# Optimization experiments

Measured on AMD Instinct MI355X. Metric: run time of the kernel, lower is better.

The kernel has to match this reference:

```python
import jax, jax.numpy as jnp
import numpy as np

B, IN, E, H, V, T = 512, 256, 256, 512, 32000, 32


def setup_inputs() -> dict:
    key = jax.random.key(0)
    ks = jax.random.split(key, 8)
    s = 0.05
    return {
        "x": jax.random.normal(ks[0], (B, IN), jnp.float32),
        "agent_w": jax.random.normal(ks[1], (H, IN), jnp.float32) * s,
        "agent_b": jnp.zeros((H,), jnp.float32),
        "sos": jax.random.normal(ks[2], (E,), jnp.float32) * 0.01,
        "emb": jax.random.normal(ks[3], (V, E), jnp.float32) * s,
        "W_ih": jax.random.normal(ks[4], (3 * H, E), jnp.float32) * s,
        "W_hh": jax.random.normal(ks[5], (3 * H, H), jnp.float32) * s,
        "b_ih": jnp.zeros((3 * H,), jnp.float32),
        "b_hh": jnp.zeros((3 * H,), jnp.float32),
        "W_out": jax.random.normal(ks[6], (V, H), jnp.float32) * s,
        "b_out": jnp.zeros((V,), jnp.float32),
        "W_stop": jax.random.normal(ks[7], (1, H), jnp.float32) * s,
        "b_stop": jnp.zeros((1,), jnp.float32),
    }


def _gru_cell(inp, h, W_ih, W_hh, b_ih, b_hh):
    gi = inp @ W_ih.T + b_ih              # [B, 3H]
    gh = h @ W_hh.T + b_hh                # [B, 3H]
    i_r, i_z, i_n = jnp.split(gi, 3, axis=1)
    h_r, h_z, h_n = jnp.split(gh, 3, axis=1)
    r = jax.nn.sigmoid(i_r + h_r)
    z = jax.nn.sigmoid(i_z + h_z)
    n = jnp.tanh(i_n + r * h_n)
    return (1.0 - z) * n + z * h


def reference(x, agent_w, agent_b, sos, emb, W_ih, W_hh, b_ih, b_hh,
              W_out, b_out, W_stop, b_stop):
    h0 = x @ agent_w.T + agent_b                       # agent(x) -> [B, H]
    inp0 = jnp.broadcast_to(sos, (x.shape[0], sos.shape[0]))
    keys = jax.random.split(jax.random.key(42), T)

    def step(carry, k):
        h, inp = carry
        h = _gru_cell(inp, h, W_ih, W_hh, b_ih, b_hh)  # noise_scale=0 -> no noise
        symb_logits = h @ W_out.T + b_out              # [B, V]
        stop_logit = (h @ W_stop.T + b_stop)[:, 0]     # [B]
        logp = jax.nn.log_softmax(symb_logits, axis=1)
        k1, k2 = jax.random.split(k)
        symb = jax.random.categorical(k1, symb_logits, axis=1)          # [B] int
        p_stop = jax.nn.sigmoid(stop_logit)
        stop = jax.random.bernoulli(k2, p_stop).astype(jnp.float32)     # [B]
        symb_lp = jnp.take_along_axis(logp, symb[:, None], axis=1)[:, 0]
        # Bernoulli: log p = s - softplus(s), log(1-p) = -softplus(s)
        sp = jax.nn.softplus(stop_logit)
        stop_lp = stop * stop_logit - sp
        symb_ent = -jnp.sum(jnp.exp(logp) * logp, axis=1)
        stop_ent = sp - stop_logit * p_stop
        inp_next = emb[symb]
        return (h, inp_next), (symb, stop, symb_lp, stop_lp, symb_ent, stop_ent)

    _, ys = jax.lax.scan(step, (h0, inp0), keys)
    symb_seq, stop_seq, symb_lp, stop_lp, symb_ent, stop_ent = ys
    # [T, B] -> [B, T]
    tr = lambda a: a.T
    return (tr(symb_seq), tr(stop_seq).astype(jnp.int32),
            tr(symb_lp), tr(stop_lp), tr(symb_ent), tr(stop_ent))
```

## Files before the change

kernel.cpp:

```cpp
#include <hip/hip_runtime.h>
#include <hip/hip_bf16.h>
#include <stdint.h>

#define JAX_PARTITIONABLE 1

#define Bz 512
#define INz 256
#define Ez 256
#define Hz 512
#define Vz 32000
#define Tz 32
#define BTz (Bz * Tz)
#define TINYF 1.17549435e-38f

typedef float otype;
__device__ __forceinline__ void store_out(otype* out, int idx, float v) {
  out[idx] = v;
}

__device__ __forceinline__ uint32_t rotl32(uint32_t x, int r) {
  return (x << r) | (x >> (32 - r));
}
__device__ __forceinline__ void threefry2x32(uint32_t k0, uint32_t k1,
                                             uint32_t x0, uint32_t x1,
                                             uint32_t& o0, uint32_t& o1) {
  const uint32_t ks2 = k0 ^ k1 ^ 0x1BD11BDAu;
  x0 += k0; x1 += k1;
#define TF_R4(a, b, c, d)                              \
  x0 += x1; x1 = rotl32(x1, a); x1 ^= x0;              \
  x0 += x1; x1 = rotl32(x1, b); x1 ^= x0;              \
  x0 += x1; x1 = rotl32(x1, c); x1 ^= x0;              \
  x0 += x1; x1 = rotl32(x1, d); x1 ^= x0;
  TF_R4(13, 15, 26, 6)  x0 += k1;  x1 += ks2 + 1u;
  TF_R4(17, 29, 16, 24) x0 += ks2; x1 += k0 + 2u;
  TF_R4(13, 15, 26, 6)  x0 += k0;  x1 += k1 + 3u;
  TF_R4(17, 29, 16, 24) x0 += k1;  x1 += ks2 + 4u;
  TF_R4(13, 15, 26, 6)  x0 += ks2; x1 += k0 + 5u;
#undef TF_R4
  o0 = x0; o1 = x1;
}
__device__ __forceinline__ uint32_t rand_bits32(uint32_t ka, uint32_t kb,
                                                uint32_t idx, uint32_t n) {
#if JAX_PARTITIONABLE
  (void)n;
  uint32_t o0, o1;
  threefry2x32(ka, kb, 0u, idx, o0, o1);
  return o0 ^ o1;
#else
  uint32_t half = n >> 1;
  uint32_t o0, o1;
  if (idx < half) { threefry2x32(ka, kb, idx, idx + half, o0, o1); return o0; }
  threefry2x32(ka, kb, idx - half, idx, o0, o1); return o1;
#endif
}
__device__ __forceinline__ float bits_to_f01(uint32_t bits) {
  return __uint_as_float((bits >> 9) | 0x3f800000u) - 1.0f;
}

__global__ void RnnSenderReinforce_36799279792759_kernel(otype* __restrict__ out,
                                                         int n, float v) {
  int i = blockIdx.x * 256 + threadIdx.x;
  if (i < n) out[i] = v;
}

__global__ void keys_kernel(uint32_t* __restrict__ keys) {
  int t = threadIdx.x;
  if (t >= Tz) return;
  uint32_t ka, kb;
#if JAX_PARTITIONABLE
  threefry2x32(0u, 42u, 0u, (uint32_t)t, ka, kb);
#else
  {
    uint32_t j0 = 2u * t, j1 = 2u * t + 1u;
    uint32_t a0, a1, b0, b1;
    if (j0 < Tz) { threefry2x32(0u, 42u, j0, j0 + Tz, a0, a1); ka = a0; }
    else         { threefry2x32(0u, 42u, j0 - Tz, j0, a0, a1); ka = a1; }
    if (j1 < Tz) { threefry2x32(0u, 42u, j1, j1 + Tz, b0, b1); kb = b0; }
    else         { threefry2x32(0u, 42u, j1 - Tz, j1, b0, b1); kb = b1; }
  }
#endif
  uint32_t o0, o1;
#if JAX_PARTITIONABLE
  threefry2x32(ka, kb, 0u, 0u, o0, o1);
  keys[t * 4 + 0] = o0; keys[t * 4 + 1] = o1;
  threefry2x32(ka, kb, 0u, 1u, o0, o1);
  keys[t * 4 + 2] = o0; keys[t * 4 + 3] = o1;
#else
  uint32_t p0, p1, q0, q1;
  threefry2x32(ka, kb, 0u, 2u, p0, p1);
  threefry2x32(ka, kb, 1u, 3u, q0, q1);
  keys[t * 4 + 0] = p0; keys[t * 4 + 1] = q0;
  keys[t * 4 + 2] = p1; keys[t * 4 + 3] = q1;
#endif
}

#define GBM 64
#define GBN 64
#define GBK 32
#define LDSS 68

__device__ __forceinline__ void gemm_bt_body(const float* __restrict__ A,
                                             const float* __restrict__ W,
                                             const float* __restrict__ bias,
                                             float* __restrict__ C,
                                             int M, int N, int K,
                                             int bx, int by,
                                             float* As, float* Bs) {
  const int tid = threadIdx.x;
  const int tx = tid & 15;
  const int ty = tid >> 4;
  const int m0 = by * GBM;
  const int n0 = bx * GBN;
  const int lr = tid >> 3;
  const int lc = (tid & 7) << 2;

  float acc[4][4] = {};
  const float* Ap = A + (size_t)(m0 + lr) * K + lc;
  const float* Wp = W + (size_t)(n0 + lr) * K + lc;
  const size_t rstep = (size_t)32 * K;

  for (int k0 = 0; k0 < K; k0 += GBK) {
    float4 a0 = *(const float4*)(Ap + k0);
    float4 a1 = *(const float4*)(Ap + k0 + rstep);
    float4 b0 = *(const float4*)(Wp + k0);
    float4 b1 = *(const float4*)(Wp + k0 + rstep);
    __syncthreads();
    As[(lc + 0) * LDSS + lr] = a0.x;
    As[(lc + 1) * LDSS + lr] = a0.y;
    As[(lc + 2) * LDSS + lr] = a0.z;
    As[(lc + 3) * LDSS + lr] = a0.w;
    As[(lc + 0) * LDSS + lr + 32] = a1.x;
    As[(lc + 1) * LDSS + lr + 32] = a1.y;
    As[(lc + 2) * LDSS + lr + 32] = a1.z;
    As[(lc + 3) * LDSS + lr + 32] = a1.w;
    Bs[(lc + 0) * LDSS + lr] = b0.x;
    Bs[(lc + 1) * LDSS + lr] = b0.y;
    Bs[(lc + 2) * LDSS + lr] = b0.z;
    Bs[(lc + 3) * LDSS + lr] = b0.w;
    Bs[(lc + 0) * LDSS + lr + 32] = b1.x;
    Bs[(lc + 1) * LDSS + lr + 32] = b1.y;
    Bs[(lc + 2) * LDSS + lr + 32] = b1.z;
    Bs[(lc + 3) * LDSS + lr + 32] = b1.w;
    __syncthreads();
#pragma unroll
    for (int kk = 0; kk < GBK; kk++) {
      float4 af = *(const float4*)&As[kk * LDSS + (ty << 2)];
      float4 bf = *(const float4*)&Bs[kk * LDSS + (tx << 2)];
      float ar[4] = {af.x, af.y, af.z, af.w};
      float br[4] = {bf.x, bf.y, bf.z, bf.w};
#pragma unroll
      for (int i = 0; i < 4; i++)
#pragma unroll
        for (int j = 0; j < 4; j++)
          acc[i][j] = fmaf(ar[i], br[j], acc[i][j]);
    }
  }

  const int nc = n0 + (tx << 2);
  float4 bv;
  bv.x = bias[nc + 0]; bv.y = bias[nc + 1]; bv.z = bias[nc + 2]; bv.w = bias[nc + 3];
#pragma unroll
  for (int i = 0; i < 4; i++) {
    int m = m0 + (ty << 2) + i;
    float4 o;
    o.x = acc[i][0] + bv.x;
    o.y = acc[i][1] + bv.y;
    o.z = acc[i][2] + bv.z;
    o.w = acc[i][3] + bv.w;
    *(float4*)(C + (size_t)m * N + nc) = o;
  }
}

__global__ __launch_bounds__(256) void gemm_bt(const float* __restrict__ A,
                                               const float* __restrict__ W,
                                               const float* __restrict__ bias,
                                               float* __restrict__ C,
                                               int M, int N, int K) {
  __shared__ __align__(16) float As[GBK * LDSS];
  __shared__ __align__(16) float Bs[GBK * LDSS];
  gemm_bt_body(A, W, bias, C, M, N, K, blockIdx.x, blockIdx.y, As, Bs);
}

__global__ __launch_bounds__(256) void gru2_kernel(const float* __restrict__ inp,
                                                   const float* __restrict__ Wih,
                                                   const float* __restrict__ bih,
                                                   float* __restrict__ gi,
                                                   const float* __restrict__ h,
                                                   const float* __restrict__ Whh,
                                                   const float* __restrict__ bhh,
                                                   float* __restrict__ gh) {
  __shared__ __align__(16) float As[GBK * LDSS];
  __shared__ __align__(16) float Bs[GBK * LDSS];
  if (blockIdx.z == 0)
    gemm_bt_body(inp, Wih, bih, gi, Bz, 3 * Hz, Ez, blockIdx.x, blockIdx.y, As, Bs);
  else
    gemm_bt_body(h, Whh, bhh, gh, Bz, 3 * Hz, Hz, blockIdx.x, blockIdx.y, As, Bs);
}

#define QBM 256
#define QBN 128
#define QBK 32
#define QLDA 260
#define QLDB 132

__global__ __launch_bounds__(512, 4) void gemm256_bt(const float* __restrict__ A,
                                                     const float* __restrict__ W,
                                                     const float* __restrict__ bias,
                                                     float* __restrict__ C,
                                                     int M, int N, int K) {
  __shared__ __align__(16) float As[QBK * QLDA];
  __shared__ __align__(16) float Bs[QBK * QLDB];
  const int tid = threadIdx.x;
  const int tx = tid & 15;
  const int ty = tid >> 4;

  const int nP = N / QBN;
  const int G = nP >> 3;
  const int lim = G << 4;
  int b = blockIdx.x;
  int P, mi;
  if (b < lim) {
    int g = b >> 4, r = b & 15;
    mi = r >> 3;
    P = (g << 3) + (r & 7);
  } else {
    int e = b - lim;
    P = (G << 3) + (e & 1);
    mi = e >> 1;
  }
  const int m0 = mi * QBM;
  const int n0 = P * QBN;

  const int ar = tid >> 1;
  const int ak = (tid & 1) << 4;
  const int br = tid >> 2;
  const int bk = (tid & 3) << 2;

  const float* Ap = A + (size_t)(m0 + ar) * K + ak;
  const float* Wp = W + (size_t)(n0 + br) * K + bk;

  float4 a0 = *(const float4*)(Ap);
  float4 a1 = *(const float4*)(Ap + 4);
  float4 a2 = *(const float4*)(Ap + 8);
  float4 a3 = *(const float4*)(Ap + 12);
  float4 b0 = *(const float4*)(Wp);
  float4 b1 = *(const float4*)(Wp + 16);

  float acc[8][8] = {};

  for (int k0 = 0; k0 < K; k0 += QBK) {
    __syncthreads();
    As[(ak + 0) * QLDA + ar] = a0.x;
    As[(ak + 1) * QLDA + ar] = a0.y;
    As[(ak + 2) * QLDA + ar] = a0.z;
    As[(ak + 3) * QLDA + ar] = a0.w;
    As[(ak + 4) * QLDA + ar] = a1.x;
    As[(ak + 5) * QLDA + ar] = a1.y;
    As[(ak + 6) * QLDA + ar] = a1.z;
    As[(ak + 7) * QLDA + ar] = a1.w;
    As[(ak + 8) * QLDA + ar] = a2.x;
    As[(ak + 9) * QLDA + ar] = a2.y;
    As[(ak + 10) * QLDA + ar] = a2.z;
    As[(ak + 11) * QLDA + ar] = a2.w;
    As[(ak + 12) * QLDA + ar] = a3.x;
    As[(ak + 13) * QLDA + ar] = a3.y;
    As[(ak + 14) * QLDA + ar] = a3.z;
    As[(ak + 15) * QLDA + ar] = a3.w;
    Bs[(bk + 0) * QLDB + br] = b0.x;
    Bs[(bk + 1) * QLDB + br] = b0.y;
    Bs[(bk + 2) * QLDB + br] = b0.z;
    Bs[(bk + 3) * QLDB + br] = b0.w;
    Bs[(16 + bk + 0) * QLDB + br] = b1.x;
    Bs[(16 + bk + 1) * QLDB + br] = b1.y;
    Bs[(16 + bk + 2) * QLDB + br] = b1.z;
    Bs[(16 + bk + 3) * QLDB + br] = b1.w;
    __syncthreads();
    if (k0 + QBK < K) {
      a0 = *(const float4*)(Ap + k0 + QBK);
      a1 = *(const float4*)(Ap + k0 + QBK + 4);
      a2 = *(const float4*)(Ap + k0 + QBK + 8);
      a3 = *(const float4*)(Ap + k0 + QBK + 12);
      b0 = *(const float4*)(Wp + k0 + QBK);
      b1 = *(const float4*)(Wp + k0 + QBK + 16);
    }
#pragma unroll 4
    for (int kk = 0; kk < QBK; kk++) {
      float4 xa0 = *(const float4*)&As[kk * QLDA + (ty << 2)];
      float4 xa1 = *(const float4*)&As[kk * QLDA + 128 + (ty << 2)];
      float4 xb0 = *(const float4*)&Bs[kk * QLDB + (tx << 2)];
      float4 xb1 = *(const float4*)&Bs[kk * QLDB + 64 + (tx << 2)];
      float ar8[8] = {xa0.x, xa0.y, xa0.z, xa0.w, xa1.x, xa1.y, xa1.z, xa1.w};
      float br8[8] = {xb0.x, xb0.y, xb0.z, xb0.w, xb1.x, xb1.y, xb1.z, xb1.w};
#pragma unroll
      for (int i = 0; i < 8; i++)
#pragma unroll
        for (int j = 0; j < 8; j++)
          acc[i][j] = fmaf(ar8[i], br8[j], acc[i][j]);
    }
  }

  const int nc0 = n0 + (tx << 2);
  const float4 bv0 = *(const float4*)(bias + nc0);
  const float4 bv1 = *(const float4*)(bias + nc0 + 64);
#pragma unroll
  for (int hf = 0; hf < 2; hf++) {
#pragma unroll
    for (int i = 0; i < 4; i++) {
      const int m = m0 + hf * 128 + (ty << 2) + i;
      float* Cp = C + (size_t)m * N + nc0;
      float4 o;
      o.x = acc[hf * 4 + i][0] + bv0.x;
      o.y = acc[hf * 4 + i][1] + bv0.y;
      o.z = acc[hf * 4 + i][2] + bv0.z;
      o.w = acc[hf * 4 + i][3] + bv0.w;
      *(float4*)Cp = o;
      float4 o2;
      o2.x = acc[hf * 4 + i][4] + bv1.x;
      o2.y = acc[hf * 4 + i][5] + bv1.y;
      o2.z = acc[hf * 4 + i][6] + bv1.z;
      o2.w = acc[hf * 4 + i][7] + bv1.w;
      *(float4*)(Cp + 64) = o2;
    }
  }
}

__global__ void gates_kernel(const float* __restrict__ gi,
                             const float* __restrict__ gh,
                             float* __restrict__ h) {
  int idx = blockIdx.x * 256 + threadIdx.x;
  int b = idx >> 9;
  int j = idx & 511;
  const float* gib = gi + (size_t)b * (3 * Hz);
  const float* ghb = gh + (size_t)b * (3 * Hz);
  float ir = gib[j], iz = gib[j + Hz], in_ = gib[j + 2 * Hz];
  float hr = ghb[j], hz = ghb[j + Hz], hn = ghb[j + 2 * Hz];
  float r = 1.0f / (1.0f + expf(-(ir + hr)));
  float z = 1.0f / (1.0f + expf(-(iz + hz)));
  float n = tanhf(in_ + r * hn);
  float hv = h[idx];
  h[idx] = (1.0f - z) * n + z * hv;
}

__global__ __launch_bounds__(256) void stop_kernel(const float* __restrict__ h,
                                                   const float* __restrict__ W_stop,
                                                   const float* __restrict__ b_stop,
                                                   const uint32_t* __restrict__ keys,
                                                   int t, otype* __restrict__ out) {
  int wave = threadIdx.x >> 6;
  int lane = threadIdx.x & 63;
  int b = blockIdx.x * 4 + wave;
  const float* hb = h + (size_t)b * Hz;
  float s = 0.0f;
  for (int k = lane; k < Hz; k += 64) s = fmaf(hb[k], W_stop[k], s);
#pragma unroll
  for (int off = 32; off; off >>= 1) s += __shfl_down(s, off, 64);
  if (lane == 0) {
    s += b_stop[0];
    uint32_t bits = rand_bits32(keys[t * 4 + 2], keys[t * 4 + 3], (uint32_t)b, Bz);
    float u = bits_to_f01(bits);
    float p = 1.0f / (1.0f + expf(-s));
    float stop = (u < p) ? 1.0f : 0.0f;
    float sp = fmaxf(s, 0.0f) + log1pf(expf(-fabsf(s)));
    store_out(out, 1 * BTz + b * Tz + t, stop);
    store_out(out, 3 * BTz + b * Tz + t, stop * s - sp);
    store_out(out, 5 * BTz + b * Tz + t, sp - s * p);
  }
}

__global__ __launch_bounds__(256) void sample_kernel(const float* __restrict__ logits,
                                                     const uint32_t* __restrict__ keys,
                                                     int t, otype* __restrict__ out,
                                                     int* __restrict__ symb_i) {
  __shared__ float sm[256], sg[256], sgl[256], sz[256], ss[256];
  __shared__ int sgi[256];
  const int tid = threadIdx.x;
  const int b = blockIdx.x;
  const float* lb = logits + (size_t)b * Vz;
  const uint32_t k1a = keys[t * 4 + 0], k1b = keys[t * 4 + 1];
  const uint32_t base = (uint32_t)b * (uint32_t)Vz;

  float m = -INFINITY, gbest = -INFINITY, glogit = 0.0f;
  int gidx = 0x7FFFFFFF;
  for (int v = tid; v < Vz; v += 256) {
    float l = lb[v];
    m = fmaxf(m, l);
    uint32_t bits = rand_bits32(k1a, k1b, base + (uint32_t)v, (uint32_t)Bz * Vz);
    float f = bits_to_f01(bits);
    float u = fmaxf(TINYF, f + TINYF);
    float g = -logf(-logf(u));
    float val = l + g;
    if (val > gbest) { gbest = val; gidx = v; glogit = l; }
  }
  sm[tid] = m; sg[tid] = gbest; sgi[tid] = gidx; sgl[tid] = glogit;
  __syncthreads();
  for (int s2 = 128; s2; s2 >>= 1) {
    if (tid < s2) {
      sm[tid] = fmaxf(sm[tid], sm[tid + s2]);
      float go = sg[tid + s2]; int io = sgi[tid + s2];
      if (go > sg[tid] || (go == sg[tid] && io < sgi[tid])) {
        sg[tid] = go; sgi[tid] = io; sgl[tid] = sgl[tid + s2];
      }
    }
    __syncthreads();
  }
  const float M = sm[0];

  float Z = 0.0f, S1 = 0.0f;
  for (int v = tid; v < Vz; v += 256) {
    float sft = lb[v] - M;
    float e = expf(sft);
    Z += e;
    S1 = fmaf(e, sft, S1);
  }
  sz[tid] = Z; ss[tid] = S1;
  __syncthreads();
  for (int s2 = 128; s2; s2 >>= 1) {
    if (tid < s2) { sz[tid] += sz[tid + s2]; ss[tid] += ss[tid + s2]; }
    __syncthreads();
  }
  if (tid == 0) {
    float Zt = sz[0], S1t = ss[0];
    float lse = logf(Zt);
    int symb = sgi[0];
    store_out(out, 0 * BTz + b * Tz + t, (float)symb);
    store_out(out, 2 * BTz + b * Tz + t, (sgl[0] - M) - lse);
    store_out(out, 4 * BTz + b * Tz + t, lse - S1t / Zt);
    symb_i[b] = symb;
  }
}

__global__ void init_inp_kernel(float* __restrict__ inp, const float* __restrict__ sos) {
  inp[blockIdx.x * Ez + threadIdx.x] = sos[threadIdx.x];
}
__global__ void gather_kernel(const float* __restrict__ emb,
                              const int* __restrict__ symb_i,
                              float* __restrict__ inp) {
  int b = blockIdx.x;
  int s = symb_i[b];
  s = (s < 0) ? 0 : ((s >= Vz) ? (Vz - 1) : s);
  inp[(size_t)b * Ez + threadIdx.x] = emb[(size_t)s * Ez + threadIdx.x];
}

extern "C" __attribute__((visibility("default")))
void kernel_launch(void* const* d_in, const int* in_sizes, int n_in,
                   void* d_out, int out_size, void* d_ws, size_t ws_size,
                   hipStream_t stream) {
  const float* x       = (const float*)d_in[0];
  const float* agent_w = (const float*)d_in[1];
  const float* agent_b = (const float*)d_in[2];
  const float* sos     = (const float*)d_in[3];
  const float* emb     = (const float*)d_in[4];
  const float* W_ih    = (const float*)d_in[5];
  const float* W_hh    = (const float*)d_in[6];
  const float* b_ih    = (const float*)d_in[7];
  const float* b_hh    = (const float*)d_in[8];
  const float* W_out   = (const float*)d_in[9];
  const float* b_out   = (const float*)d_in[10];
  const float* W_stop  = (const float*)d_in[11];
  const float* b_stop  = (const float*)d_in[12];
  otype* out = (otype*)d_out;

  float* ws = (float*)d_ws;
  float* h      = ws;
  float* inp    = h + (size_t)Bz * Hz;
  float* gi     = inp + (size_t)Bz * Ez;
  float* gh     = gi + (size_t)Bz * 3 * Hz;
  float* logits = gh + (size_t)Bz * 3 * Hz;
  int* symb_i   = (int*)(logits + (size_t)Bz * Vz);
  uint32_t* keys = (uint32_t*)(symb_i + Bz);

  keys_kernel<<<1, 64, 0, stream>>>(keys);
  init_inp_kernel<<<Bz, Ez, 0, stream>>>(inp, sos);
  gemm_bt<<<dim3(Hz / GBN, Bz / GBM), 256, 0, stream>>>(x, agent_w, agent_b, h,
                                                        Bz, Hz, INz);
  for (int t = 0; t < Tz; t++) {
    gru2_kernel<<<dim3(3 * Hz / GBN, Bz / GBM, 2), 256, 0, stream>>>(
        inp, W_ih, b_ih, gi, h, W_hh, b_hh, gh);
    gates_kernel<<<(Bz * Hz) / 256, 256, 0, stream>>>(gi, gh, h);
    gemm256_bt<<<(Vz / QBN) * (Bz / QBM), 512, 0, stream>>>(h, W_out, b_out,
                                                            logits, Bz, Vz, Hz);
    stop_kernel<<<Bz / 4, 256, 0, stream>>>(h, W_stop, b_stop, keys, t, out);
    sample_kernel<<<Bz, 256, 0, stream>>>(logits, keys, t, out, symb_i);
    gather_kernel<<<Bz, Ez, 0, stream>>>(emb, symb_i, inp);
  }
}
```

Measured before the change: 10.82 ms.

## Enlarge output GEMM per-thread tile and fuse gates/stop and sample/gather kernels

The vocab-projection GEMM now runs with 256 threads per block, each computing a 16x8 accumulator tile instead of 8x8, so LDS traffic per FMA drops. The cost is higher register pressure and fewer resident waves. The GRU gate update is fused with the stop-logit computation, with the new hidden row kept in shared memory. The embedding gather is folded into the sampling kernel, which removes two launches per timestep and the symb_i round trip through global memory.

After: 11.12 ms. 2.8% more time.

```diff
diff --git a/kernel.cpp b/kernel.cpp
--- a/kernel.cpp
+++ b/kernel.cpp
@@ -203,7 +203,7 @@
 #define QLDA 260
 #define QLDB 132
 
-__global__ __launch_bounds__(512, 4) void gemm256_bt(const float* __restrict__ A,
+__global__ __launch_bounds__(256, 2) void gemm256_bt(const float* __restrict__ A,
                                                      const float* __restrict__ W,
                                                      const float* __restrict__ bias,
                                                      float* __restrict__ C,
@@ -231,71 +231,61 @@
   const int m0 = mi * QBM;
   const int n0 = P * QBN;
 
-  const int ar = tid >> 1;
-  const int ak = (tid & 1) << 4;
-  const int br = tid >> 2;
-  const int bk = (tid & 3) << 2;
-
-  const float* Ap = A + (size_t)(m0 + ar) * K + ak;
-  const float* Wp = W + (size_t)(n0 + br) * K + bk;
-
-  float4 a0 = *(const float4*)(Ap);
-  float4 a1 = *(const float4*)(Ap + 4);
-  float4 a2 = *(const float4*)(Ap + 8);
-  float4 a3 = *(const float4*)(Ap + 12);
-  float4 b0 = *(const float4*)(Wp);
-  float4 b1 = *(const float4*)(Wp + 16);
-
-  float acc[8][8] = {};
+  const float* Ap = A + (size_t)(m0 + tid) * K;
+  const int brr = tid >> 1;
+  const int bk = (tid & 1) << 4;
+  const float* Wp = W + (size_t)(n0 + brr) * K + bk;
+
+  float4 a[8], bb[4];
+#pragma unroll
+  for (int j = 0; j < 8; j++) a[j] = *(const float4*)(Ap + j * 4);
+#pragma unroll
+  for (int j = 0; j < 4; j++) bb[j] = *(const float4*)(Wp + j * 4);
+
+  float acc[16][8] = {};
 
   for (int k0 = 0; k0 < K; k0 += QBK) {
     __syncthreads();
-    As[(ak + 0) * QLDA + ar] = a0.x;
-    As[(ak + 1) * QLDA + ar] = a0.y;
-    As[(ak + 2) * QLDA + ar] = a0.z;
-    As[(ak + 3) * QLDA + ar] = a0.w;
-    As[(ak + 4) * QLDA + ar] = a1.x;
-    As[(ak + 5) * QLDA + ar] = a1.y;
-    As[(ak + 6) * QLDA + ar] = a1.z;
-    As[(ak + 7) * QLDA + ar] = a1.w;
-    As[(ak + 8) * QLDA + ar] = a2.x;
-    As[(ak + 9) * QLDA + ar] = a2.y;
-    As[(ak + 10) * QLDA + ar] = a2.z;
-    As[(ak + 11) * QLDA + ar] = a2.w;
-    As[(ak + 12) * QLDA + ar] = a3.x;
-    As[(ak + 13) * QLDA + ar] = a3.y;
-    As[(ak + 14) * QLDA + ar] = a3.z;
-    As[(ak + 15) * QLDA + ar] = a3.w;
-    Bs[(bk + 0) * QLDB + br] = b0.x;
-    Bs[(bk + 1) * QLDB + br] = b0.y;
-    Bs[(bk + 2) * QLDB + br] = b0.z;
-    Bs[(bk + 3) * QLDB + br] = b0.w;
-    Bs[(16 + bk + 0) * QLDB + br] = b1.x;
-    Bs[(16 + bk + 1) * QLDB + br] = b1.y;
-    Bs[(16 + bk + 2) * QLDB + br] = b1.z;
-    Bs[(16 + bk + 3) * QLDB + br] = b1.w;
+#pragma unroll
+    for (int j = 0; j < 8; j++) {
+      As[(j * 4 + 0) * QLDA + tid] = a[j].x;
+      As[(j * 4 + 1) * QLDA + tid] = a[j].y;
+      As[(j * 4 + 2) * QLDA + tid] = a[j].z;
+      As[(j * 4 + 3) * QLDA + tid] = a[j].w;
+    }
+#pragma unroll
+    for (int j = 0; j < 4; j++) {
+      Bs[(bk + j * 4 + 0) * QLDB + brr] = bb[j].x;
+      Bs[(bk + j * 4 + 1) * QLDB + brr] = bb[j].y;
+      Bs[(bk + j * 4 + 2) * QLDB + brr] = bb[j].z;
+      Bs[(bk + j * 4 + 3) * QLDB + brr] = bb[j].w;
+    }
     __syncthreads();
     if (k0 + QBK < K) {
-      a0 = *(const float4*)(Ap + k0 + QBK);
-      a1 = *(const float4*)(Ap + k0 + QBK + 4);
-      a2 = *(const float4*)(Ap + k0 + QBK + 8);
-      a3 = *(const float4*)(Ap + k0 + QBK + 12);
-      b0 = *(const float4*)(Wp + k0 + QBK);
-      b1 = *(const float4*)(Wp + k0 + QBK + 16);
-    }
-#pragma unroll 4
+#pragma unroll
+      for (int j = 0; j < 8; j++)
+        a[j] = *(const float4*)(Ap + k0 + QBK + j * 4);
+#pragma unroll
+      for (int j = 0; j < 4; j++)
+        bb[j] = *(const float4*)(Wp + k0 + QBK + j * 4);
+    }
+#pragma unroll 2
     for (int kk = 0; kk < QBK; kk++) {
-      float4 xa0 = *(const float4*)&As[kk * QLDA + (ty << 2)];
-      float4 xa1 = *(const float4*)&As[kk * QLDA + 128 + (ty << 2)];
+      const float* Ar = &As[kk * QLDA + (ty << 2)];
+      float4 xa0 = *(const float4*)(Ar);
+      float4 xa1 = *(const float4*)(Ar + 64);
+      float4 xa2 = *(const float4*)(Ar + 128);
+      float4 xa3 = *(const float4*)(Ar + 192);
       float4 xb0 = *(const float4*)&Bs[kk * QLDB + (tx << 2)];
       float4 xb1 = *(const float4*)&Bs[kk * QLDB + 64 + (tx << 2)];
-      float ar8[8] = {xa0.x, xa0.y, xa0.z, xa0.w, xa1.x, xa1.y, xa1.z, xa1.w};
-      float br8[8] = {xb0.x, xb0.y, xb0.z, xb0.w, xb1.x, xb1.y, xb1.z, xb1.w};
-#pragma unroll
-      for (int i = 0; i < 8; i++)
+      float am[16] = {xa0.x, xa0.y, xa0.z, xa0.w, xa1.x, xa1.y, xa1.z, xa1.w,
+                      xa2.x, xa2.y, xa2.z, xa2.w, xa3.x, xa3.y, xa3.z, xa3.w};
+      float bn[8] = {xb0.x, xb0.y, xb0.z, xb0.w, xb1.x, xb1.y, xb1.z, xb1.w};
+#pragma unroll
+      for (int i = 0; i < 16; i++)
 #pragma unroll
         for (int j = 0; j < 8; j++)
-          acc[i][j] = fmaf(ar8[i], br8[j], acc[i][j]);
+          acc[i][j] = fmaf(am[i], bn[j], acc[i][j]);
     }
   }
 
@@ -303,33 +293,35 @@
   const float4 bv0 = *(const float4*)(bias + nc0);
   const float4 bv1 = *(const float4*)(bias + nc0 + 64);
 #pragma unroll
-  for (int hf = 0; hf < 2; hf++) {
+  for (int q = 0; q < 4; q++) {
 #pragma unroll
     for (int i = 0; i < 4; i++) {
-      const int m = m0 + hf * 128 + (ty << 2) + i;
+      const int m = m0 + q * 64 + (ty << 2) + i;
       float* Cp = C + (size_t)m * N + nc0;
       float4 o;
-      o.x = acc[hf * 4 + i][0] + bv0.x;
-      o.y = acc[hf * 4 + i][1] + bv0.y;
-      o.z = acc[hf * 4 + i][2] + bv0.z;
-      o.w = acc[hf * 4 + i][3] + bv0.w;
+      o.x = acc[q * 4 + i][0] + bv0.x;
+      o.y = acc[q * 4 + i][1] + bv0.y;
+      o.z = acc[q * 4 + i][2] + bv0.z;
+      o.w = acc[q * 4 + i][3] + bv0.w;
       *(float4*)Cp = o;
       float4 o2;
-      o2.x = acc[hf * 4 + i][4] + bv1.x;
-      o2.y = acc[hf * 4 + i][5] + bv1.y;
-      o2.z = acc[hf * 4 + i][6] + bv1.z;
-      o2.w = acc[hf * 4 + i][7] + bv1.w;
+      o2.x = acc[q * 4 + i][4] + bv1.x;
+      o2.y = acc[q * 4 + i][5] + bv1.y;
+      o2.z = acc[q * 4 + i][6] + bv1.z;
+      o2.w = acc[q * 4 + i][7] + bv1.w;
       *(float4*)(Cp + 64) = o2;
     }
   }
 }
 
-__global__ void gates_kernel(const float* __restrict__ gi,
-                             const float* __restrict__ gh,
-                             float* __restrict__ h) {
-  int idx = blockIdx.x * 256 + threadIdx.x;
-  int b = idx >> 9;
-  int j = idx & 511;
+__global__ __launch_bounds__(512) void gates_stop_kernel(
+    const float* __restrict__ gi, const float* __restrict__ gh,
+    float* __restrict__ h, const float* __restrict__ W_stop,
+    const float* __restrict__ b_stop, const uint32_t* __restrict__ keys,
+    int t, otype* __restrict__ out) {
+  __shared__ float hrow[Hz];
+  const int b = blockIdx.x;
+  const int j = threadIdx.x;
   const float* gib = gi + (size_t)b * (3 * Hz);
   const float* ghb = gh + (size_t)b * (3 * Hz);
   float ir = gib[j], iz = gib[j + Hz], in_ = gib[j + 2 * Hz];
@@ -337,42 +329,39 @@
   float r = 1.0f / (1.0f + expf(-(ir + hr)));
   float z = 1.0f / (1.0f + expf(-(iz + hz)));
   float n = tanhf(in_ + r * hn);
-  float hv = h[idx];
-  h[idx] = (1.0f - z) * n + z * hv;
-}
-
-__global__ __launch_bounds__(256) void stop_kernel(const float* __restrict__ h,
-                                                   const float* __restrict__ W_stop,
-                                                   const float* __restrict__ b_stop,
-                                                   const uint32_t* __restrict__ keys,
-                                                   int t, otype* __restrict__ out) {
-  int wave = threadIdx.x >> 6;
-  int lane = threadIdx.x & 63;
-  int b = blockIdx.x * 4 + wave;
-  const float* hb = h + (size_t)b * Hz;
-  float s = 0.0f;
-  for (int k = lane; k < Hz; k += 64) s = fmaf(hb[k], W_stop[k], s);
-#pragma unroll
-  for (int off = 32; off; off >>= 1) s += __shfl_down(s, off, 64);
-  if (lane == 0) {
-    s += b_stop[0];
-    uint32_t bits = rand_bits32(keys[t * 4 + 2], keys[t * 4 + 3], (uint32_t)b, Bz);
-    float u = bits_to_f01(bits);
-    float p = 1.0f / (1.0f + expf(-s));
-    float stop = (u < p) ? 1.0f : 0.0f;
-    float sp = fmaxf(s, 0.0f) + log1pf(expf(-fabsf(s)));
-    store_out(out, 1 * BTz + b * Tz + t, stop);
-    store_out(out, 3 * BTz + b * Tz + t, stop * s - sp);
-    store_out(out, 5 * BTz + b * Tz + t, sp - s * p);
+  float hv = h[(size_t)b * Hz + j];
+  float hnew = (1.0f - z) * n + z * hv;
+  h[(size_t)b * Hz + j] = hnew;
+  hrow[j] = hnew;
+  __syncthreads();
+  if (j < 64) {
+    const int lane = j;
+    float s = 0.0f;
+    for (int k = lane; k < Hz; k += 64) s = fmaf(hrow[k], W_stop[k], s);
+#pragma unroll
+    for (int off = 32; off; off >>= 1) s += __shfl_down(s, off, 64);
+    if (lane == 0) {
+      s += b_stop[0];
+      uint32_t bits = rand_bits32(keys[t * 4 + 2], keys[t * 4 + 3], (uint32_t)b, Bz);
+      float u = bits_to_f01(bits);
+      float p = 1.0f / (1.0f + expf(-s));
+      float stop = (u < p) ? 1.0f : 0.0f;
+      float sp = fmaxf(s, 0.0f) + log1pf(expf(-fabsf(s)));
+      store_out(out, 1 * BTz + b * Tz + t, stop);
+      store_out(out, 3 * BTz + b * Tz + t, stop * s - sp);
+      store_out(out, 5 * BTz + b * Tz + t, sp - s * p);
+    }
   }
 }
 
 __global__ __launch_bounds__(256) void sample_kernel(const float* __restrict__ logits,
                                                      const uint32_t* __restrict__ keys,
                                                      int t, otype* __restrict__ out,
-                                                     int* __restrict__ symb_i) {
+                                                     const float* __restrict__ emb,
+                                                     float* __restrict__ inp) {
   __shared__ float sm[256], sg[256], sgl[256], sz[256], ss[256];
   __shared__ int sgi[256];
+  __shared__ int ssymb;
   const int tid = threadIdx.x;
   const int b = blockIdx.x;
   const float* lb = logits + (size_t)b * Vz;
@@ -425,20 +414,16 @@
     store_out(out, 0 * BTz + b * Tz + t, (float)symb);
     store_out(out, 2 * BTz + b * Tz + t, (sgl[0] - M) - lse);
     store_out(out, 4 * BTz + b * Tz + t, lse - S1t / Zt);
-    symb_i[b] = symb;
-  }
+    ssymb = symb;
+  }
+  __syncthreads();
+  int s = ssymb;
+  s = (s < 0) ? 0 : ((s >= Vz) ? (Vz - 1) : s);
+  inp[(size_t)b * Ez + tid] = emb[(size_t)s * Ez + tid];
 }
 
 __global__ void init_inp_kernel(float* __restrict__ inp, const float* __restrict__ sos) {
   inp[blockIdx.x * Ez + threadIdx.x] = sos[threadIdx.x];
-}
-__global__ void gather_kernel(const float* __restrict__ emb,
-                              const int* __restrict__ symb_i,
-                              float* __restrict__ inp) {
-  int b = blockIdx.x;
-  int s = symb_i[b];
-  s = (s < 0) ? 0 : ((s >= Vz) ? (Vz - 1) : s);
-  inp[(size_t)b * Ez + threadIdx.x] = emb[(size_t)s * Ez + threadIdx.x];
 }
 
 extern "C" __attribute__((visibility("default")))
@@ -466,8 +451,7 @@
   float* gi     = inp + (size_t)Bz * Ez;
   float* gh     = gi + (size_t)Bz * 3 * Hz;
   float* logits = gh + (size_t)Bz * 3 * Hz;
-  int* symb_i   = (int*)(logits + (size_t)Bz * Vz);
-  uint32_t* keys = (uint32_t*)(symb_i + Bz);
+  uint32_t* keys = (uint32_t*)(logits + (size_t)Bz * Vz);
 
   keys_kernel<<<1, 64, 0, stream>>>(keys);
   init_inp_kernel<<<Bz, Ez, 0, stream>>>(inp, sos);
@@ -476,11 +460,10 @@
   for (int t = 0; t < Tz; t++) {
     gru2_kernel<<<dim3(3 * Hz / GBN, Bz / GBM, 2), 256, 0, stream>>>(
         inp, W_ih, b_ih, gi, h, W_hh, b_hh, gh);
-    gates_kernel<<<(Bz * Hz) / 256, 256, 0, stream>>>(gi, gh, h);
-    gemm256_bt<<<(Vz / QBN) * (Bz / QBM), 512, 0, stream>>>(h, W_out, b_out,
+    gates_stop_kernel<<<Bz, 512, 0, stream>>>(gi, gh, h, W_stop, b_stop, keys,
+                                              t, out);
+    gemm256_bt<<<(Vz / QBN) * (Bz / QBM), 256, 0, stream>>>(h, W_out, b_out,
                                                             logits, Bz, Vz, Hz);
-    stop_kernel<<<Bz / 4, 256, 0, stream>>>(h, W_stop, b_stop, keys, t, out);
-    sample_kernel<<<Bz, 256, 0, stream>>>(logits, keys, t, out, symb_i);
-    gather_kernel<<<Bz, Ez, 0, stream>>>(emb, symb_i, inp);
-  }
-}
+    sample_kernel<<<Bz, 256, 0, stream>>>(logits, keys, t, out, emb, inp);
+  }
+}
```
